# Optimization experiments

Measured on AMD Instinct MI355X. Metric: run time of the kernel, lower is better.

The kernel has to match this reference:

```python
import jax, jax.numpy as jnp
import numpy as np

N_NODES = 20000
N_EDGES = 320000
NUM_GRAPHS = 64
IN_DIM = 256


def setup_inputs() -> dict:
    key = jax.random.key(0)
    ks = jax.random.split(key, 12)
    x = jax.random.normal(ks[0], (N_NODES, IN_DIM), dtype=jnp.float32)
    edge_index = jax.random.randint(ks[1], (2, N_EDGES), 0, N_NODES, dtype=jnp.int64)
    batch = jnp.sort(jax.random.randint(ks[2], (N_NODES,), 0, NUM_GRAPHS, dtype=jnp.int64))
    def glorot(k, shape):
        lim = float(np.sqrt(6.0 / (shape[0] + shape[1])))
        return jax.random.uniform(k, shape, dtype=jnp.float32, minval=-lim, maxval=lim)
    W1 = glorot(ks[3], (IN_DIM, 256)); b1 = jnp.zeros((256,), jnp.float32)
    W2 = glorot(ks[4], (256, 128));   b2 = jnp.zeros((128,), jnp.float32)
    Wl1 = glorot(ks[5], (128, 64));   bl1 = jnp.zeros((64,), jnp.float32)
    Wl2 = glorot(ks[6], (64, 1));     bl2 = jnp.zeros((1,), jnp.float32)
    return {"x": x, "edge_index": edge_index, "batch": batch,
            "W1": W1, "b1": b1, "W2": W2, "b2": b2,
            "Wl1": Wl1, "bl1": bl1, "Wl2": Wl2, "bl2": bl2}


def gcn_conv(x, src, dst, W, b, n_nodes):
    # PyG GCNConv: add self-loops, symmetric normalization D^-1/2 (A+I) D^-1/2,
    # linear transform first, then gather-scale-scatter aggregation, then bias.
    loop = jnp.arange(n_nodes, dtype=src.dtype)
    s = jnp.concatenate([src, loop])
    d = jnp.concatenate([dst, loop])
    deg = jax.ops.segment_sum(jnp.ones_like(d, dtype=x.dtype), d, num_segments=n_nodes)
    dinv = jnp.where(deg > 0, jax.lax.rsqrt(deg), 0.0)
    norm = dinv[s] * dinv[d]                         # [E+N]
    h = x @ W                                        # [N, out]
    msg = h[s] * norm[:, None]                       # [E+N, out]
    out = jax.ops.segment_sum(msg, d, num_segments=n_nodes)
    return out + b


def global_mean_pool(x, batch, num_graphs):
    sums = jax.ops.segment_sum(x, batch, num_segments=num_graphs)
    cnts = jax.ops.segment_sum(jnp.ones((x.shape[0],), x.dtype), batch, num_segments=num_graphs)
    return sums / jnp.maximum(cnts, 1.0)[:, None]


def reference(x, edge_index, batch, W1, b1, W2, b2, Wl1, bl1, Wl2, bl2):
    n = x.shape[0]
    src, dst = edge_index[0], edge_index[1]
    h = jax.nn.relu(gcn_conv(x, src, dst, W1, b1, n))   # dropout = identity (eval)
    h = jax.nn.relu(gcn_conv(h, src, dst, W2, b2, n))
    g = global_mean_pool(h, batch, NUM_GRAPHS)          # [G, 128]
    g = jax.nn.relu(g @ Wl1 + bl1)
    return jax.nn.sigmoid(g @ Wl2 + bl2)                # [G, 1]
```

## Files before the change

kernel.cpp:

```cpp
#include <hip/hip_runtime.h>
#include <hip/hip_bf16.h>
#include <math.h>

typedef __attribute__((ext_vector_type(8))) short bf16x8;
typedef __attribute__((ext_vector_type(4))) float f32x4;

__device__ __forceinline__ unsigned short f2bf(float f) {
    unsigned int u = __float_as_uint(f);
    unsigned int r = (u + 0x7FFFu + ((u >> 16) & 1u)) >> 16;
    return (unsigned short)r;
}
__device__ __forceinline__ unsigned char f2fp8(float v) {
    int p = __builtin_amdgcn_cvt_pk_fp8_f32(v, v, 0, false);
    return (unsigned char)(p & 0xff);
}
__device__ __forceinline__ unsigned int pk4fp8(float a, float b, float c, float d) {
    int p = __builtin_amdgcn_cvt_pk_fp8_f32(a, b, 0, false);
    p = __builtin_amdgcn_cvt_pk_fp8_f32(c, d, p, true);
    return (unsigned int)p;
}
__device__ __forceinline__ void fp8x8_fma(uint2 u, float w, float* a) {
    a[0] += __builtin_amdgcn_cvt_f32_fp8((int)u.x, 0) * w;
    a[1] += __builtin_amdgcn_cvt_f32_fp8((int)u.x, 1) * w;
    a[2] += __builtin_amdgcn_cvt_f32_fp8((int)u.x, 2) * w;
    a[3] += __builtin_amdgcn_cvt_f32_fp8((int)u.x, 3) * w;
    a[4] += __builtin_amdgcn_cvt_f32_fp8((int)u.y, 0) * w;
    a[5] += __builtin_amdgcn_cvt_f32_fp8((int)u.y, 1) * w;
    a[6] += __builtin_amdgcn_cvt_f32_fp8((int)u.y, 2) * w;
    a[7] += __builtin_amdgcn_cvt_f32_fp8((int)u.y, 3) * w;
}
__device__ __forceinline__ void fp8x4_fma(unsigned int u, float w, float* a) {
    a[0] += __builtin_amdgcn_cvt_f32_fp8((int)u, 0) * w;
    a[1] += __builtin_amdgcn_cvt_f32_fp8((int)u, 1) * w;
    a[2] += __builtin_amdgcn_cvt_f32_fp8((int)u, 2) * w;
    a[3] += __builtin_amdgcn_cvt_f32_fp8((int)u, 3) * w;
}
__device__ __forceinline__ float deg_dinv(int c) { return rsqrtf((float)c + 1.0f); }

__device__ __forceinline__ void load_lds16(const unsigned short* g, unsigned short* l) {
    __builtin_amdgcn_global_load_lds(
        (const __attribute__((address_space(1))) unsigned int*)g,
        (__attribute__((address_space(3))) unsigned int*)l, 16, 0, 0);
}

__global__ __launch_bounds__(256) void prep_kernel(const float* __restrict__ x,
                                                   unsigned short* __restrict__ xh,
                                                   const int* __restrict__ batch,
                                                   int* __restrict__ gstart,
                                                   const float* __restrict__ W1,
                                                   unsigned short* __restrict__ w1t,
                                                   const float* __restrict__ W2,
                                                   unsigned short* __restrict__ w2t,
                                                   int N, int G, int CXB, int BNB) {
    int b = blockIdx.x;
    int tid = threadIdx.x;
    if (b < CXB) {
        size_t idx0 = ((size_t)b * 256 + tid) * 2;
        size_t total4 = (size_t)N * 64;
#pragma unroll
        for (int r = 0; r < 2; r++) {
            size_t idx = idx0 + r;
            if (idx < total4) {
                float4 v = ((const float4*)x)[idx];
                ushort4 o;
                o.x = f2bf(v.x); o.y = f2bf(v.y); o.z = f2bf(v.z); o.w = f2bf(v.w);
                ((ushort4*)xh)[idx] = o;
            }
        }
        return;
    }
    b -= CXB;
    if (b < BNB) {
        int i = b * 256 + tid;
        if (i >= N) return;
        int bb = batch[i];
        if (i == 0) { for (int g = 0; g <= bb; g++) gstart[g] = 0; }
        else { int bp = batch[i - 1]; for (int g = bp + 1; g <= bb; g++) gstart[g] = i; }
        if (i == N - 1) { for (int g = bb + 1; g <= G; g++) gstart[g] = N; }
        return;
    }
    b -= BNB;
    {
        int idx = b * 256 + tid;
        if (idx < 256 * 256) {
            int m = idx >> 8, k = idx & 255;
            w1t[idx] = f2bf(W1[(size_t)k * 256 + m]);
        } else if (idx < 256 * 256 + 128 * 256) {
            int j = idx - 256 * 256;
            int m = j >> 8, k = j & 255;
            w2t[j] = f2bf(W2[(size_t)k * 128 + m]);
        }
    }
}

__device__ __forceinline__ void gemm_body(const unsigned short* __restrict__ A,
                                          const unsigned short* __restrict__ Bt,
                                          unsigned char* __restrict__ C8,
                                          int N, int M, int bx, int by,
                                          unsigned short* As, unsigned short* Bs) {
    const int K = 256;
    int tid = threadIdx.x;
    int wave = tid >> 6, lane = tid & 63;
    int quad = lane >> 4, m16 = lane & 15;
    int r0 = by * 128, c0 = bx * 64;
    int srow = lane >> 2;
    int skoff = (lane & 3) * 8;

    f32x4 acc[2][4];
#pragma unroll
    for (int rg = 0; rg < 2; rg++)
#pragma unroll
        for (int ct = 0; ct < 4; ct++) acc[rg][ct] = (f32x4){0.f, 0.f, 0.f, 0.f};

    for (int kb = 0; kb < K; kb += 32) {
#pragma unroll
        for (int i = 0; i < 2; i++) {
            int brow = wave * 32 + i * 16 + srow;
            int grow = r0 + brow; if (grow >= N) grow = N - 1;
            load_lds16(A + (size_t)grow * K + kb + skoff, As + (wave * 32 + i * 16) * 32);
        }
        {
            int bcol = wave * 16 + srow;
            load_lds16(Bt + (size_t)(c0 + bcol) * K + kb + skoff, Bs + (wave * 16) * 32);
        }
        __syncthreads();
        bf16x8 af[2], bf[4];
#pragma unroll
        for (int rg = 0; rg < 2; rg++)
            af[rg] = *(const bf16x8*)(As + (wave * 32 + rg * 16 + m16) * 32 + quad * 8);
#pragma unroll
        for (int ct = 0; ct < 4; ct++)
            bf[ct] = *(const bf16x8*)(Bs + (ct * 16 + m16) * 32 + quad * 8);
#pragma unroll
        for (int rg = 0; rg < 2; rg++)
#pragma unroll
            for (int ct = 0; ct < 4; ct++)
                acc[rg][ct] = __builtin_amdgcn_mfma_f32_16x16x32_bf16(af[rg], bf[ct], acc[rg][ct], 0, 0, 0);
        __syncthreads();
    }
#pragma unroll
    for (int rg = 0; rg < 2; rg++) {
#pragma unroll
        for (int ct = 0; ct < 4; ct++) {
            int col = c0 + ct * 16 + m16;
#pragma unroll
            for (int r = 0; r < 4; r++) {
                int row = r0 + wave * 32 + rg * 16 + quad * 4 + r;
                if (row < N) C8[(size_t)row * M + col] = f2fp8(acc[rg][ct][r]);
            }
        }
    }
}

__global__ __launch_bounds__(256) void fill_gemm1_kernel(const int* __restrict__ src,
                                                         const int* __restrict__ dst,
                                                         int* __restrict__ cnt,
                                                         int* __restrict__ csr,
                                                         const unsigned short* __restrict__ A,
                                                         const unsigned short* __restrict__ Bt,
                                                         unsigned char* __restrict__ C8,
                                                         int N, int E, int FB) {
    __shared__ unsigned short As[128 * 32];
    __shared__ unsigned short Bs[64 * 32];
    if ((int)blockIdx.x < FB) {
        int e = (blockIdx.x * 256 + threadIdx.x) * 4;
        if (e + 3 < E) {
            int4 d4 = *(const int4*)(dst + e);
            int4 s4 = *(const int4*)(src + e);
            int sl;
            sl = atomicAdd(&cnt[d4.x], 1); if (sl < 64) csr[(d4.x << 6) + sl] = s4.x;
            sl = atomicAdd(&cnt[d4.y], 1); if (sl < 64) csr[(d4.y << 6) + sl] = s4.y;
            sl = atomicAdd(&cnt[d4.z], 1); if (sl < 64) csr[(d4.z << 6) + sl] = s4.z;
            sl = atomicAdd(&cnt[d4.w], 1); if (sl < 64) csr[(d4.w << 6) + sl] = s4.w;
        } else {
            for (; e < E; e++) {
                int d = dst[e];
                int slot = atomicAdd(&cnt[d], 1);
                if (slot < 64) csr[(d << 6) + slot] = src[e];
            }
        }
        return;
    }
    int gb = blockIdx.x - FB;
    gemm_body(A, Bt, C8, N, 256, gb & 3, gb >> 2, As, Bs);
}

__global__ __launch_bounds__(256) void gemm2_kernel(const unsigned short* __restrict__ A,
                                                    const unsigned short* __restrict__ Bt,
                                                    unsigned char* __restrict__ C8, int N) {
    __shared__ unsigned short As[128 * 32];
    __shared__ unsigned short Bs[64 * 32];
    gemm_body(A, Bt, C8, N, 128, blockIdx.x, blockIdx.y, As, Bs);
}

__global__ __launch_bounds__(256) void gather256_kernel(const unsigned char* __restrict__ h8,
                                                        const int* __restrict__ csr,
                                                        const int* __restrict__ cnt,
                                                        const float* __restrict__ bias,
                                                        unsigned short* __restrict__ out, int N) {
    int node = blockIdx.x * 4 + (threadIdx.x >> 6);
    if (node >= N) return;
    int lane = threadIdx.x & 63;
    int half = lane >> 5, hl = lane & 31;
    int beg = node << 6;
    int c = cnt[node]; if (c > 64) c = 64;
    int end = beg + c;
    float a[8] = {0, 0, 0, 0, 0, 0, 0, 0};
    int j = beg;
    for (; j + 7 < end; j += 8) {
        int s0 = csr[j + half], s1 = csr[j + 2 + half];
        int s2 = csr[j + 4 + half], s3 = csr[j + 6 + half];
        float w0 = deg_dinv(cnt[s0]), w1 = deg_dinv(cnt[s1]);
        float w2 = deg_dinv(cnt[s2]), w3 = deg_dinv(cnt[s3]);
        uint2 u0 = *(const uint2*)(h8 + (size_t)s0 * 256 + hl * 8);
        uint2 u1 = *(const uint2*)(h8 + (size_t)s1 * 256 + hl * 8);
        uint2 u2 = *(const uint2*)(h8 + (size_t)s2 * 256 + hl * 8);
        uint2 u3 = *(const uint2*)(h8 + (size_t)s3 * 256 + hl * 8);
        fp8x8_fma(u0, w0, a); fp8x8_fma(u1, w1, a);
        fp8x8_fma(u2, w2, a); fp8x8_fma(u3, w3, a);
    }
    for (; j + 1 < end; j += 2) {
        int s0 = csr[j + half];
        float w0 = deg_dinv(cnt[s0]);
        uint2 u0 = *(const uint2*)(h8 + (size_t)s0 * 256 + hl * 8);
        fp8x8_fma(u0, w0, a);
    }
    if (j < end && half == 0) {
        int s0 = csr[j];
        float w0 = deg_dinv(cnt[s0]);
        uint2 u0 = *(const uint2*)(h8 + (size_t)s0 * 256 + hl * 8);
        fp8x8_fma(u0, w0, a);
    }
#pragma unroll
    for (int i = 0; i < 8; i++) a[i] += __shfl_down(a[i], 32);
    if (half == 0) {
        float dd = deg_dinv(c);
        float self[8] = {0, 0, 0, 0, 0, 0, 0, 0};
        uint2 uh = *(const uint2*)(h8 + (size_t)node * 256 + hl * 8);
        fp8x8_fma(uh, dd, self);
        float4 bv0 = ((const float4*)bias)[hl * 2];
        float4 bv1 = ((const float4*)bias)[hl * 2 + 1];
        float bvf[8] = {bv0.x, bv0.y, bv0.z, bv0.w, bv1.x, bv1.y, bv1.z, bv1.w};
        bf16x8 o;
#pragma unroll
        for (int i = 0; i < 8; i++)
            o[i] = (short)f2bf(fmaxf((a[i] + self[i]) * dd + bvf[i], 0.f));
        ((bf16x8*)(out + (size_t)node * 256))[hl] = o;
    }
}

__global__ __launch_bounds__(256) void gather128_kernel(const unsigned char* __restrict__ t8,
                                                        const int* __restrict__ csr,
                                                        const int* __restrict__ cnt,
                                                        const float* __restrict__ bias,
                                                        unsigned char* __restrict__ out2, int N) {
    int node = blockIdx.x * 4 + (threadIdx.x >> 6);
    if (node >= N) return;
    int lane = threadIdx.x & 63;
    int half = lane >> 5, hl = lane & 31;
    int beg = node << 6;
    int c = cnt[node]; if (c > 64) c = 64;
    int end = beg + c;
    float a[4] = {0, 0, 0, 0};
    int j = beg;
    for (; j + 7 < end; j += 8) {
        int s0 = csr[j + half], s1 = csr[j + 2 + half];
        int s2 = csr[j + 4 + half], s3 = csr[j + 6 + half];
        float w0 = deg_dinv(cnt[s0]), w1 = deg_dinv(cnt[s1]);
        float w2 = deg_dinv(cnt[s2]), w3 = deg_dinv(cnt[s3]);
        unsigned int u0 = *(const unsigned int*)(t8 + (size_t)s0 * 128 + hl * 4);
        unsigned int u1 = *(const unsigned int*)(t8 + (size_t)s1 * 128 + hl * 4);
        unsigned int u2 = *(const unsigned int*)(t8 + (size_t)s2 * 128 + hl * 4);
        unsigned int u3 = *(const unsigned int*)(t8 + (size_t)s3 * 128 + hl * 4);
        fp8x4_fma(u0, w0, a); fp8x4_fma(u1, w1, a);
        fp8x4_fma(u2, w2, a); fp8x4_fma(u3, w3, a);
    }
    for (; j + 1 < end; j += 2) {
        int s0 = csr[j + half];
        float w0 = deg_dinv(cnt[s0]);
        unsigned int u0 = *(const unsigned int*)(t8 + (size_t)s0 * 128 + hl * 4);
        fp8x4_fma(u0, w0, a);
    }
    if (j < end && half == 0) {
        int s0 = csr[j];
        float w0 = deg_dinv(cnt[s0]);
        unsigned int u0 = *(const unsigned int*)(t8 + (size_t)s0 * 128 + hl * 4);
        fp8x4_fma(u0, w0, a);
    }
#pragma unroll
    for (int i = 0; i < 4; i++) a[i] += __shfl_down(a[i], 32);
    if (half == 0) {
        float dd = deg_dinv(c);
        float self[4] = {0, 0, 0, 0};
        unsigned int uh = *(const unsigned int*)(t8 + (size_t)node * 128 + hl * 4);
        fp8x4_fma(uh, dd, self);
        float4 bv = ((const float4*)bias)[hl];
        float r0 = fmaxf((a[0] + self[0]) * dd + bv.x, 0.f);
        float r1 = fmaxf((a[1] + self[1]) * dd + bv.y, 0.f);
        float r2 = fmaxf((a[2] + self[2]) * dd + bv.z, 0.f);
        float r3 = fmaxf((a[3] + self[3]) * dd + bv.w, 0.f);
        ((unsigned int*)(out2 + (size_t)node * 128))[hl] = pk4fp8(r0, r1, r2, r3);
    }
}

__global__ __launch_bounds__(256) void poolhead_kernel(const unsigned char* __restrict__ out2,
                                                       const int* __restrict__ gstart,
                                                       float* __restrict__ gsum,
                                                       int* __restrict__ gdone,
                                                       const float* __restrict__ Wl1,
                                                       const float* __restrict__ bl1,
                                                       const float* __restrict__ Wl2,
                                                       const float* __restrict__ bl2,
                                                       float* __restrict__ out) {
    int g = blockIdx.x >> 3, slice = blockIdx.x & 7;
    int tid = threadIdx.x;
    int hw = tid >> 5, hl = tid & 31;
    int gs = gstart[g], ge = gstart[g + 1];
    float a[4] = {0, 0, 0, 0};
    for (int i = gs + slice * 8 + hw; i < ge; i += 64) {
        unsigned int u = ((const unsigned int*)(out2 + (size_t)i * 128))[hl];
        fp8x4_fma(u, 1.0f, a);
    }
    __shared__ float red[8][128];
#pragma unroll
    for (int k = 0; k < 4; k++) red[hw][hl * 4 + k] = a[k];
    __syncthreads();
    if (tid < 128) {
        float s = 0.f;
#pragma unroll
        for (int w = 0; w < 8; w++) s += red[w][tid];
        if (s != 0.f) atomicAdd(&gsum[g * 128 + tid], s);
    }
    __syncthreads();
    __shared__ int lastflag;
    if (tid == 0) {
        __threadfence();
        int old = atomicAdd(&gdone[g], 1);
        lastflag = (old == 7) ? 1 : 0;
    }
    __syncthreads();
    if (!lastflag) return;
    __shared__ float gv[128];
    if (tid < 128) {
        float s = atomicAdd(&gsum[g * 128 + tid], 0.0f);
        float cntf = fmaxf((float)(ge - gs), 1.0f);
        gv[tid] = s / cntf;
    }
    __syncthreads();
    if (tid < 64) {
        float acc = bl1[tid];
#pragma unroll 8
        for (int k = 0; k < 128; k++) acc += gv[k] * Wl1[k * 64 + tid];
        acc = fmaxf(acc, 0.f);
        float p = acc * Wl2[tid];
#pragma unroll
        for (int off = 32; off; off >>= 1) p += __shfl_down(p, off);
        if (tid == 0) out[g] = 1.f / (1.f + expf(-(p + bl2[0])));
    }
}

extern "C" void kernel_launch(void* const* d_in, const int* in_sizes, int n_in,
                              void* d_out, int out_size, void* d_ws, size_t ws_size,
                              hipStream_t stream) {
    const float* x   = (const float*)d_in[0];
    const int* ei    = (const int*)d_in[1];
    const int* batch = (const int*)d_in[2];
    const float* W1  = (const float*)d_in[3];
    const float* b1  = (const float*)d_in[4];
    const float* W2  = (const float*)d_in[5];
    const float* b2  = (const float*)d_in[6];
    const float* Wl1 = (const float*)d_in[7];
    const float* bl1 = (const float*)d_in[8];
    const float* Wl2 = (const float*)d_in[9];
    const float* bl2 = (const float*)d_in[10];
    float* out = (float*)d_out;

    const int N = in_sizes[2];
    const int E = in_sizes[1] / 2;
    const int G = 64;
    const int* src = ei;
    const int* dst = ei + E;

    char* base = (char*)d_ws;
    size_t off = 0;
    auto carve = [&](size_t bytes) -> char* {
        char* p = base + off;
        off = (off + bytes + 15) & ~(size_t)15;
        return p;
    };
    int*   cnt    = (int*)carve((size_t)N * 4);
    float* gsum   = (float*)carve((size_t)G * 128 * 4);
    int*   gdone  = (int*)carve((size_t)G * 4);
    size_t zero_bytes = (size_t)(N + G * 128 + G) * 4 + 32;
    int*   csr    = (int*)carve((size_t)N * 64 * 4);
    int*   gstart = (int*)carve((size_t)(G + 1) * 4);
    unsigned short* w1t = (unsigned short*)carve((size_t)256 * 256 * 2);
    unsigned short* w2t = (unsigned short*)carve((size_t)128 * 256 * 2);
    unsigned short* xh  = (unsigned short*)carve((size_t)N * 256 * 2);
    unsigned char*  h8  = (unsigned char*)carve((size_t)N * 256);
    unsigned short* o1h = (unsigned short*)carve((size_t)N * 256 * 2);
    unsigned char* t8   = (unsigned char*)xh;
    unsigned char* out2 = h8;

    hipMemsetAsync(d_ws, 0, zero_bytes, stream);

    const int CXB = (int)(((size_t)N * 32 + 255) / 256);
    const int BNB = (N + 255) / 256;
    const int CWB = (256 * 256 + 128 * 256 + 255) / 256;
    prep_kernel<<<CXB + BNB + CWB, 256, 0, stream>>>(
        x, xh, batch, gstart, W1, w1t, W2, w2t, N, G, CXB, BNB);

    const int FB  = (E / 4 + 255) / 256;
    const int GB1 = 4 * ((N + 127) / 128);
    fill_gemm1_kernel<<<FB + GB1, 256, 0, stream>>>(src, dst, cnt, csr,
                                                    xh, w1t, h8, N, E, FB);

    gather256_kernel<<<(N + 3) / 4, 256, 0, stream>>>(h8, csr, cnt, b1, o1h, N);

    {
        dim3 grid(2, (N + 127) / 128);
        gemm2_kernel<<<grid, 256, 0, stream>>>(o1h, w2t, t8, N);
    }
    gather128_kernel<<<(N + 3) / 4, 256, 0, stream>>>(t8, csr, cnt, b2, out2, N);

    poolhead_kernel<<<G * 8, 256, 0, stream>>>(out2, gstart, gsum, gdone,
                                               Wl1, bl1, Wl2, bl2, out);
}
```

Measured before the change: 173.4 us.

## Fuse x conversion into GEMM1, use FP8 for layer-2 GEMM, fuse pooling into gather

Drops the separate fp32-to-bf16 pass over x. GEMM1 now reads fp32 x directly, converts it in registers and writes a swizzled LDS tile, with the output tile widened to 128 columns. Layer-1 output is stored as FP8 instead of bf16, and GEMM2 uses FP8 MFMA with half-size loads. The second gather is fused with mean pooling and the MLP head: per-graph partial sums are accumulated with atomics, and a per-graph completion counter lets the last block finish the head. This removes one kernel launch and a full pass over the activations, but adds more quantization error and atomic contention.

```diff
diff --git a/kernel.cpp b/kernel.cpp
--- a/kernel.cpp
+++ b/kernel.cpp
@@ -42,34 +42,21 @@
         (const __attribute__((address_space(1))) unsigned int*)g,
         (__attribute__((address_space(3))) unsigned int*)l, 16, 0, 0);
 }
-
-__global__ __launch_bounds__(256) void prep_kernel(const float* __restrict__ x,
-                                                   unsigned short* __restrict__ xh,
-                                                   const int* __restrict__ batch,
+__device__ __forceinline__ void load_lds16_u8(const unsigned char* g, unsigned char* l) {
+    __builtin_amdgcn_global_load_lds(
+        (const __attribute__((address_space(1))) unsigned int*)g,
+        (__attribute__((address_space(3))) unsigned int*)l, 16, 0, 0);
+}
+
+__global__ __launch_bounds__(256) void prep_kernel(const int* __restrict__ batch,
                                                    int* __restrict__ gstart,
                                                    const float* __restrict__ W1,
                                                    unsigned short* __restrict__ w1t,
                                                    const float* __restrict__ W2,
-                                                   unsigned short* __restrict__ w2t,
-                                                   int N, int G, int CXB, int BNB) {
+                                                   unsigned char* __restrict__ w2t8,
+                                                   int N, int G, int BNB) {
     int b = blockIdx.x;
     int tid = threadIdx.x;
-    if (b < CXB) {
-        size_t idx0 = ((size_t)b * 256 + tid) * 2;
-        size_t total4 = (size_t)N * 64;
-#pragma unroll
-        for (int r = 0; r < 2; r++) {
-            size_t idx = idx0 + r;
-            if (idx < total4) {
-                float4 v = ((const float4*)x)[idx];
-                ushort4 o;
-                o.x = f2bf(v.x); o.y = f2bf(v.y); o.z = f2bf(v.z); o.w = f2bf(v.w);
-                ((ushort4*)xh)[idx] = o;
-            }
-        }
-        return;
-    }
-    b -= CXB;
     if (b < BNB) {
         int i = b * 256 + tid;
         if (i >= N) return;
@@ -79,76 +66,14 @@
         if (i == N - 1) { for (int g = bb + 1; g <= G; g++) gstart[g] = N; }
         return;
     }
-    b -= BNB;
-    {
-        int idx = b * 256 + tid;
-        if (idx < 256 * 256) {
-            int m = idx >> 8, k = idx & 255;
-            w1t[idx] = f2bf(W1[(size_t)k * 256 + m]);
-        } else if (idx < 256 * 256 + 128 * 256) {
-            int j = idx - 256 * 256;
-            int m = j >> 8, k = j & 255;
-            w2t[j] = f2bf(W2[(size_t)k * 128 + m]);
-        }
-    }
-}
-
-__device__ __forceinline__ void gemm_body(const unsigned short* __restrict__ A,
-                                          const unsigned short* __restrict__ Bt,
-                                          unsigned char* __restrict__ C8,
-                                          int N, int M, int bx, int by,
-                                          unsigned short* As, unsigned short* Bs) {
-    const int K = 256;
-    int tid = threadIdx.x;
-    int wave = tid >> 6, lane = tid & 63;
-    int quad = lane >> 4, m16 = lane & 15;
-    int r0 = by * 128, c0 = bx * 64;
-    int srow = lane >> 2;
-    int skoff = (lane & 3) * 8;
-
-    f32x4 acc[2][4];
-#pragma unroll
-    for (int rg = 0; rg < 2; rg++)
-#pragma unroll
-        for (int ct = 0; ct < 4; ct++) acc[rg][ct] = (f32x4){0.f, 0.f, 0.f, 0.f};
-
-    for (int kb = 0; kb < K; kb += 32) {
-#pragma unroll
-        for (int i = 0; i < 2; i++) {
-            int brow = wave * 32 + i * 16 + srow;
-            int grow = r0 + brow; if (grow >= N) grow = N - 1;
-            load_lds16(A + (size_t)grow * K + kb + skoff, As + (wave * 32 + i * 16) * 32);
-        }
-        {
-            int bcol = wave * 16 + srow;
-            load_lds16(Bt + (size_t)(c0 + bcol) * K + kb + skoff, Bs + (wave * 16) * 32);
-        }
-        __syncthreads();
-        bf16x8 af[2], bf[4];
-#pragma unroll
-        for (int rg = 0; rg < 2; rg++)
-            af[rg] = *(const bf16x8*)(As + (wave * 32 + rg * 16 + m16) * 32 + quad * 8);
-#pragma unroll
-        for (int ct = 0; ct < 4; ct++)
-            bf[ct] = *(const bf16x8*)(Bs + (ct * 16 + m16) * 32 + quad * 8);
-#pragma unroll
-        for (int rg = 0; rg < 2; rg++)
-#pragma unroll
-            for (int ct = 0; ct < 4; ct++)
-                acc[rg][ct] = __builtin_amdgcn_mfma_f32_16x16x32_bf16(af[rg], bf[ct], acc[rg][ct], 0, 0, 0);
-        __syncthreads();
-    }
-#pragma unroll
-    for (int rg = 0; rg < 2; rg++) {
-#pragma unroll
-        for (int ct = 0; ct < 4; ct++) {
-            int col = c0 + ct * 16 + m16;
-#pragma unroll
-            for (int r = 0; r < 4; r++) {
-                int row = r0 + wave * 32 + rg * 16 + quad * 4 + r;
-                if (row < N) C8[(size_t)row * M + col] = f2fp8(acc[rg][ct][r]);
-            }
-        }
+    int idx = (b - BNB) * 256 + tid;
+    if (idx < 256 * 256) {
+        int m = idx >> 8, k = idx & 255;
+        w1t[idx] = f2bf(W1[(size_t)k * 256 + m]);
+    } else if (idx < 256 * 256 + 128 * 256) {
+        int j = idx - 256 * 256;
+        int m = j >> 8, k = j & 255;
+        w2t8[j] = f2fp8(W2[(size_t)k * 128 + m]);
     }
 }
 
@@ -156,12 +81,12 @@
                                                          const int* __restrict__ dst,
                                                          int* __restrict__ cnt,
                                                          int* __restrict__ csr,
-                                                         const unsigned short* __restrict__ A,
+                                                         const float* __restrict__ x,
                                                          const unsigned short* __restrict__ Bt,
                                                          unsigned char* __restrict__ C8,
                                                          int N, int E, int FB) {
     __shared__ unsigned short As[128 * 32];
-    __shared__ unsigned short Bs[64 * 32];
+    __shared__ unsigned short Bs[128 * 32];
     if ((int)blockIdx.x < FB) {
         int e = (blockIdx.x * 256 + threadIdx.x) * 4;
         if (e + 3 < E) {
@@ -182,22 +107,141 @@
         return;
     }
     int gb = blockIdx.x - FB;
-    gemm_body(A, Bt, C8, N, 256, gb & 3, gb >> 2, As, Bs);
-}
-
-__global__ __launch_bounds__(256) void gemm2_kernel(const unsigned short* __restrict__ A,
-                                                    const unsigned short* __restrict__ Bt,
+    int bx = gb & 1, by = gb >> 1;
+    const int K = 256;
+    int tid = threadIdx.x;
+    int wave = tid >> 6, lane = tid & 63;
+    int quad = lane >> 4, m16 = lane & 15;
+    int r0 = by * 128, c0 = bx * 128;
+    int srow = lane >> 2;
+    int skoff = (lane & 3) * 8;
+
+    f32x4 acc[2][8];
+#pragma unroll
+    for (int rg = 0; rg < 2; rg++)
+#pragma unroll
+        for (int ct = 0; ct < 8; ct++) acc[rg][ct] = (f32x4){0.f, 0.f, 0.f, 0.f};
+
+    int arow = tid >> 1, akh = tid & 1;
+    int agrow = r0 + arow; if (agrow >= N) agrow = N - 1;
+    const float* ap = x + (size_t)agrow * K + akh * 16;
+    int asw = (arow >> 1) & 3;
+    unsigned short* as0 = As + arow * 32 + ((((akh << 1) | 0) ^ asw) << 3);
+    unsigned short* as1 = As + arow * 32 + ((((akh << 1) | 1) ^ asw) << 3);
+    int rsw = (m16 >> 1) & 3;
+
+    for (int kb = 0; kb < K; kb += 32) {
+        float4 f0 = *(const float4*)(ap + kb);
+        float4 f1 = *(const float4*)(ap + kb + 4);
+        float4 f2 = *(const float4*)(ap + kb + 8);
+        float4 f3 = *(const float4*)(ap + kb + 12);
+        {
+            int bcol = wave * 16 + srow;
+            load_lds16(Bt + (size_t)(c0 + bcol) * K + kb + skoff, Bs + (wave * 16) * 32);
+            load_lds16(Bt + (size_t)(c0 + 64 + bcol) * K + kb + skoff, Bs + (64 + wave * 16) * 32);
+        }
+        bf16x8 u0, u1;
+        u0[0] = (short)f2bf(f0.x); u0[1] = (short)f2bf(f0.y);
+        u0[2] = (short)f2bf(f0.z); u0[3] = (short)f2bf(f0.w);
+        u0[4] = (short)f2bf(f1.x); u0[5] = (short)f2bf(f1.y);
+        u0[6] = (short)f2bf(f1.z); u0[7] = (short)f2bf(f1.w);
+        u1[0] = (short)f2bf(f2.x); u1[1] = (short)f2bf(f2.y);
+        u1[2] = (short)f2bf(f2.z); u1[3] = (short)f2bf(f2.w);
+        u1[4] = (short)f2bf(f3.x); u1[5] = (short)f2bf(f3.y);
+        u1[6] = (short)f2bf(f3.z); u1[7] = (short)f2bf(f3.w);
+        *(bf16x8*)as0 = u0;
+        *(bf16x8*)as1 = u1;
+        __syncthreads();
+        bf16x8 af[2], bfr[8];
+#pragma unroll
+        for (int rg = 0; rg < 2; rg++)
+            af[rg] = *(const bf16x8*)(As + (wave * 32 + rg * 16 + m16) * 32 + ((quad ^ rsw) << 3));
+#pragma unroll
+        for (int ct = 0; ct < 8; ct++)
+            bfr[ct] = *(const bf16x8*)(Bs + (ct * 16 + m16) * 32 + (quad << 3));
+#pragma unroll
+        for (int rg = 0; rg < 2; rg++)
+#pragma unroll
+            for (int ct = 0; ct < 8; ct++)
+                acc[rg][ct] = __builtin_amdgcn_mfma_f32_16x16x32_bf16(af[rg], bfr[ct], acc[rg][ct], 0, 0, 0);
+        __syncthreads();
+    }
+#pragma unroll
+    for (int rg = 0; rg < 2; rg++) {
+#pragma unroll
+        for (int ct = 0; ct < 8; ct++) {
+            int col = c0 + ct * 16 + m16;
+#pragma unroll
+            for (int r = 0; r < 4; r++) {
+                int row = r0 + wave * 32 + rg * 16 + quad * 4 + r;
+                if (row < N) C8[(size_t)row * 256 + col] = f2fp8(acc[rg][ct][r]);
+            }
+        }
+    }
+}
+
+__global__ __launch_bounds__(256) void gemm2_kernel(const unsigned char* __restrict__ A,
+                                                    const unsigned char* __restrict__ Bt,
                                                     unsigned char* __restrict__ C8, int N) {
-    __shared__ unsigned short As[128 * 32];
-    __shared__ unsigned short Bs[64 * 32];
-    gemm_body(A, Bt, C8, N, 128, blockIdx.x, blockIdx.y, As, Bs);
+    __shared__ unsigned char As8[128 * 32];
+    __shared__ unsigned char Bs8[64 * 32];
+    const int K = 256;
+    int tid = threadIdx.x;
+    int wave = tid >> 6, lane = tid & 63;
+    int quad = lane >> 4, m16 = lane & 15;
+    int bx = blockIdx.x, by = blockIdx.y;
+    int r0 = by * 128, c0 = bx * 64;
+
+    f32x4 acc[2][4];
+#pragma unroll
+    for (int rg = 0; rg < 2; rg++)
+#pragma unroll
+        for (int ct = 0; ct < 4; ct++) acc[rg][ct] = (f32x4){0.f, 0.f, 0.f, 0.f};
+
+    int arow = wave * 32 + (lane >> 1);
+    int agrow = r0 + arow; if (agrow >= N) agrow = N - 1;
+    int ach = (lane & 1) * 16;
+    int brow = (wave & 1) * 32 + (lane >> 1);
+    int bch = (lane & 1) * 16;
+
+    for (int kb = 0; kb < K; kb += 32) {
+        load_lds16_u8(A + (size_t)agrow * K + kb + ach, As8 + (wave * 32) * 32);
+        if (wave < 2)
+            load_lds16_u8(Bt + (size_t)(c0 + brow) * K + kb + bch, Bs8 + (wave * 32) * 32);
+        __syncthreads();
+        long af[2], bfr[4];
+#pragma unroll
+        for (int rg = 0; rg < 2; rg++)
+            af[rg] = *(const long*)(As8 + (wave * 32 + rg * 16 + m16) * 32 + (quad << 3));
+#pragma unroll
+        for (int ct = 0; ct < 4; ct++)
+            bfr[ct] = *(const long*)(Bs8 + (ct * 16 + m16) * 32 + (quad << 3));
+#pragma unroll
+        for (int rg = 0; rg < 2; rg++)
+#pragma unroll
+            for (int ct = 0; ct < 4; ct++)
+                acc[rg][ct] = __builtin_amdgcn_mfma_f32_16x16x32_fp8_fp8(af[rg], bfr[ct], acc[rg][ct], 0, 0, 0);
+        __syncthreads();
+    }
+#pragma unroll
+    for (int rg = 0; rg < 2; rg++) {
+#pragma unroll
+        for (int ct = 0; ct < 4; ct++) {
+            int col = c0 + ct * 16 + m16;
+#pragma unroll
+            for (int r = 0; r < 4; r++) {
+                int row = r0 + wave * 32 + rg * 16 + quad * 4 + r;
+                if (row < N) C8[(size_t)row * 128 + col] = f2fp8(acc[rg][ct][r]);
+            }
+        }
+    }
 }
 
 __global__ __launch_bounds__(256) void gather256_kernel(const unsigned char* __restrict__ h8,
                                                         const int* __restrict__ csr,
                                                         const int* __restrict__ cnt,
                                                         const float* __restrict__ bias,
-                                                        unsigned short* __restrict__ out, int N) {
+                                                        unsigned char* __restrict__ o18, int N) {
     int node = blockIdx.x * 4 + (threadIdx.x >> 6);
     if (node >= N) return;
     int lane = threadIdx.x & 63;
@@ -241,121 +285,152 @@
         float4 bv0 = ((const float4*)bias)[hl * 2];
         float4 bv1 = ((const float4*)bias)[hl * 2 + 1];
         float bvf[8] = {bv0.x, bv0.y, bv0.z, bv0.w, bv1.x, bv1.y, bv1.z, bv1.w};
-        bf16x8 o;
-#pragma unroll
-        for (int i = 0; i < 8; i++)
-            o[i] = (short)f2bf(fmaxf((a[i] + self[i]) * dd + bvf[i], 0.f));
-        ((bf16x8*)(out + (size_t)node * 256))[hl] = o;
-    }
-}
-
-__global__ __launch_bounds__(256) void gather128_kernel(const unsigned char* __restrict__ t8,
-                                                        const int* __restrict__ csr,
-                                                        const int* __restrict__ cnt,
-                                                        const float* __restrict__ bias,
-                                                        unsigned char* __restrict__ out2, int N) {
-    int node = blockIdx.x * 4 + (threadIdx.x >> 6);
-    if (node >= N) return;
-    int lane = threadIdx.x & 63;
+        float v[8];
+#pragma unroll
+        for (int i = 0; i < 8; i++) v[i] = fmaxf((a[i] + self[i]) * dd + bvf[i], 0.f);
+        uint2 o;
+        o.x = pk4fp8(v[0], v[1], v[2], v[3]);
+        o.y = pk4fp8(v[4], v[5], v[6], v[7]);
+        ((uint2*)(o18 + (size_t)node * 256))[hl] = o;
+    }
+}
+
+__global__ __launch_bounds__(256) void gather128ph_kernel(const unsigned char* __restrict__ t8,
+                                                          const int* __restrict__ csr,
+                                                          const int* __restrict__ cnt,
+                                                          const float* __restrict__ bias,
+                                                          const int* __restrict__ batch,
+                                                          const int* __restrict__ gstart,
+                                                          float* __restrict__ gsum,
+                                                          int* __restrict__ gdone,
+                                                          const float* __restrict__ Wl1,
+                                                          const float* __restrict__ bl1,
+                                                          const float* __restrict__ Wl2,
+                                                          const float* __restrict__ bl2,
+                                                          float* __restrict__ out, int N) {
+    int tid = threadIdx.x;
+    int nw = tid >> 6;
+    int node = blockIdx.x * 4 + nw;
+    int lane = tid & 63;
     int half = lane >> 5, hl = lane & 31;
-    int beg = node << 6;
-    int c = cnt[node]; if (c > 64) c = 64;
-    int end = beg + c;
-    float a[4] = {0, 0, 0, 0};
-    int j = beg;
-    for (; j + 7 < end; j += 8) {
-        int s0 = csr[j + half], s1 = csr[j + 2 + half];
-        int s2 = csr[j + 4 + half], s3 = csr[j + 6 + half];
-        float w0 = deg_dinv(cnt[s0]), w1 = deg_dinv(cnt[s1]);
-        float w2 = deg_dinv(cnt[s2]), w3 = deg_dinv(cnt[s3]);
-        unsigned int u0 = *(const unsigned int*)(t8 + (size_t)s0 * 128 + hl * 4);
-        unsigned int u1 = *(const unsigned int*)(t8 + (size_t)s1 * 128 + hl * 4);
-        unsigned int u2 = *(const unsigned int*)(t8 + (size_t)s2 * 128 + hl * 4);
-        unsigned int u3 = *(const unsigned int*)(t8 + (size_t)s3 * 128 + hl * 4);
-        fp8x4_fma(u0, w0, a); fp8x4_fma(u1, w1, a);
-        fp8x4_fma(u2, w2, a); fp8x4_fma(u3, w3, a);
-    }
-    for (; j + 1 < end; j += 2) {
-        int s0 = csr[j + half];
-        float w0 = deg_dinv(cnt[s0]);
-        unsigned int u0 = *(const unsigned int*)(t8 + (size_t)s0 * 128 + hl * 4);
-        fp8x4_fma(u0, w0, a);
-    }
-    if (j < end && half == 0) {
-        int s0 = csr[j];
-        float w0 = deg_dinv(cnt[s0]);
-        unsigned int u0 = *(const unsigned int*)(t8 + (size_t)s0 * 128 + hl * 4);
-        fp8x4_fma(u0, w0, a);
-    }
-#pragma unroll
-    for (int i = 0; i < 4; i++) a[i] += __shfl_down(a[i], 32);
-    if (half == 0) {
-        float dd = deg_dinv(c);
-        float self[4] = {0, 0, 0, 0};
-        unsigned int uh = *(const unsigned int*)(t8 + (size_t)node * 128 + hl * 4);
-        fp8x4_fma(uh, dd, self);
-        float4 bv = ((const float4*)bias)[hl];
-        float r0 = fmaxf((a[0] + self[0]) * dd + bv.x, 0.f);
-        float r1 = fmaxf((a[1] + self[1]) * dd + bv.y, 0.f);
-        float r2 = fmaxf((a[2] + self[2]) * dd + bv.z, 0.f);
-        float r3 = fmaxf((a[3] + self[3]) * dd + bv.w, 0.f);
-        ((unsigned int*)(out2 + (size_t)node * 128))[hl] = pk4fp8(r0, r1, r2, r3);
-    }
-}
-
-__global__ __launch_bounds__(256) void poolhead_kernel(const unsigned char* __restrict__ out2,
-                                                       const int* __restrict__ gstart,
-                                                       float* __restrict__ gsum,
-                                                       int* __restrict__ gdone,
-                                                       const float* __restrict__ Wl1,
-                                                       const float* __restrict__ bl1,
-                                                       const float* __restrict__ Wl2,
-                                                       const float* __restrict__ bl2,
-                                                       float* __restrict__ out) {
-    int g = blockIdx.x >> 3, slice = blockIdx.x & 7;
-    int tid = threadIdx.x;
-    int hw = tid >> 5, hl = tid & 31;
-    int gs = gstart[g], ge = gstart[g + 1];
-    float a[4] = {0, 0, 0, 0};
-    for (int i = gs + slice * 8 + hw; i < ge; i += 64) {
-        unsigned int u = ((const unsigned int*)(out2 + (size_t)i * 128))[hl];
-        fp8x4_fma(u, 1.0f, a);
-    }
-    __shared__ float red[8][128];
-#pragma unroll
-    for (int k = 0; k < 4; k++) red[hw][hl * 4 + k] = a[k];
+    bool valid = node < N;
+
+    __shared__ float red[4][128];
+    __shared__ int gid[4];
+    __shared__ int fg[4];
+    __shared__ int nf;
+    __shared__ float gv[128];
+
+    if (valid) {
+        int beg = node << 6;
+        int c = cnt[node]; if (c > 64) c = 64;
+        int end = beg + c;
+        float a[4] = {0, 0, 0, 0};
+        int j = beg;
+        for (; j + 7 < end; j += 8) {
+            int s0 = csr[j + half], s1 = csr[j + 2 + half];
+            int s2 = csr[j + 4 + half], s3 = csr[j + 6 + half];
+            float w0 = deg_dinv(cnt[s0]), w1 = deg_dinv(cnt[s1]);
+            float w2 = deg_dinv(cnt[s2]), w3 = deg_dinv(cnt[s3]);
+            unsigned int u0 = *(const unsigned int*)(t8 + (size_t)s0 * 128 + hl * 4);
+            unsigned int u1 = *(const unsigned int*)(t8 + (size_t)s1 * 128 + hl * 4);
+            unsigned int u2 = *(const unsigned int*)(t8 + (size_t)s2 * 128 + hl * 4);
+            unsigned int u3 = *(const unsigned int*)(t8 + (size_t)s3 * 128 + hl * 4);
+            fp8x4_fma(u0, w0, a); fp8x4_fma(u1, w1, a);
+            fp8x4_fma(u2, w2, a); fp8x4_fma(u3, w3, a);
+        }
+        for (; j + 1 < end; j += 2) {
+            int s0 = csr[j + half];
+            float w0 = deg_dinv(cnt[s0]);
+            unsigned int u0 = *(const unsigned int*)(t8 + (size_t)s0 * 128 + hl * 4);
+            fp8x4_fma(u0, w0, a);
+        }
+        if (j < end && half == 0) {
+            int s0 = csr[j];
+            float w0 = deg_dinv(cnt[s0]);
+            unsigned int u0 = *(const unsigned int*)(t8 + (size_t)s0 * 128 + hl * 4);
+            fp8x4_fma(u0, w0, a);
+        }
+#pragma unroll
+        for (int i = 0; i < 4; i++) a[i] += __shfl_down(a[i], 32);
+        if (lane == 0) gid[nw] = batch[node];
+        if (half == 0) {
+            float dd = deg_dinv(c);
+            float self[4] = {0, 0, 0, 0};
+            unsigned int uh = *(const unsigned int*)(t8 + (size_t)node * 128 + hl * 4);
+            fp8x4_fma(uh, dd, self);
+            float4 bv = ((const float4*)bias)[hl];
+            red[nw][hl * 4 + 0] = fmaxf((a[0] + self[0]) * dd + bv.x, 0.f);
+            red[nw][hl * 4 + 1] = fmaxf((a[1] + self[1]) * dd + bv.y, 0.f);
+            red[nw][hl * 4 + 2] = fmaxf((a[2] + self[2]) * dd + bv.z, 0.f);
+            red[nw][hl * 4 + 3] = fmaxf((a[3] + self[3]) * dd + bv.w, 0.f);
+        }
+    } else {
+        if (lane == 0) gid[nw] = -1;
+    }
     __syncthreads();
     if (tid < 128) {
-        float s = 0.f;
-#pragma unroll
-        for (int w = 0; w < 8; w++) s += red[w][tid];
-        if (s != 0.f) atomicAdd(&gsum[g * 128 + tid], s);
+        float s = 0.f; int gp = -1;
+#pragma unroll
+        for (int n = 0; n < 4; n++) {
+            int g = gid[n];
+            if (g < 0) continue;
+            if (g != gp) {
+                if (gp >= 0 && s != 0.f) atomicAdd(&gsum[gp * 128 + tid], s);
+                s = 0.f; gp = g;
+            }
+            s += red[n][tid];
+        }
+        if (gp >= 0 && s != 0.f) atomicAdd(&gsum[gp * 128 + tid], s);
     }
     __syncthreads();
-    __shared__ int lastflag;
     if (tid == 0) {
+        nf = 0;
         __threadfence();
-        int old = atomicAdd(&gdone[g], 1);
-        lastflag = (old == 7) ? 1 : 0;
+        int n = 0;
+        while (n < 4) {
+            int g = gid[n];
+            if (g < 0) { n++; continue; }
+            int len = 1;
+            while (n + len < 4 && gid[n + len] == g) len++;
+            int tot = gstart[g + 1] - gstart[g];
+            int old = atomicAdd(&gdone[g], len);
+            if (old + len == tot) fg[nf++] = g;
+            n += len;
+        }
     }
     __syncthreads();
-    if (!lastflag) return;
-    __shared__ float gv[128];
-    if (tid < 128) {
-        float s = atomicAdd(&gsum[g * 128 + tid], 0.0f);
-        float cntf = fmaxf((float)(ge - gs), 1.0f);
-        gv[tid] = s / cntf;
-    }
-    __syncthreads();
-    if (tid < 64) {
-        float acc = bl1[tid];
+    int nfl = nf;
+    for (int f = 0; f < nfl; f++) {
+        int g = fg[f];
+        if (tid < 128) {
+            float s = atomicAdd(&gsum[g * 128 + tid], 0.0f);
+            float cf = fmaxf((float)(gstart[g + 1] - gstart[g]), 1.0f);
+            gv[tid] = s / cf;
+        }
+        __syncthreads();
+        if (tid < 64) {
+            float acc = bl1[tid];
 #pragma unroll 8
-        for (int k = 0; k < 128; k++) acc += gv[k] * Wl1[k * 64 + tid];
-        acc = fmaxf(acc, 0.f);
-        float p = acc * Wl2[tid];
-#pragma unroll
-        for (int off = 32; off; off >>= 1) p += __shfl_down(p, off);
-        if (tid == 0) out[g] = 1.f / (1.f + expf(-(p + bl2[0])));
+            for (int k = 0; k < 128; k++) acc += gv[k] * Wl1[k * 64 + tid];
+            acc = fmaxf(acc, 0.f);
+            float p = acc * Wl2[tid];
+#pragma unroll
+            for (int off = 32; off; off >>= 1) p += __shfl_down(p, off);
+            if (tid == 0) out[g] = 1.f / (1.f + expf(-(p + bl2[0])));
+        }
+        __syncthreads();
+    }
+    if (blockIdx.x == 0 && tid < 64) {
+        for (int g = 0; g < 64; g++) {
+            if (gstart[g + 1] == gstart[g]) {
+                float acc = fmaxf(bl1[tid], 0.f);
+                float p = acc * Wl2[tid];
+#pragma unroll
+                for (int off = 32; off; off >>= 1) p += __shfl_down(p, off);
+                if (tid == 0) out[g] = 1.f / (1.f + expf(-(p + bl2[0])));
+            }
+        }
     }
 }
 
@@ -394,35 +469,30 @@
     size_t zero_bytes = (size_t)(N + G * 128 + G) * 4 + 32;
     int*   csr    = (int*)carve((size_t)N * 64 * 4);
     int*   gstart = (int*)carve((size_t)(G + 1) * 4);
-    unsigned short* w1t = (unsigned short*)carve((size_t)256 * 256 * 2);
-    unsigned short* w2t = (unsigned short*)carve((size_t)128 * 256 * 2);
-    unsigned short* xh  = (unsigned short*)carve((size_t)N * 256 * 2);
-    unsigned char*  h8  = (unsigned char*)carve((size_t)N * 256);
-    unsigned short* o1h = (unsigned short*)carve((size_t)N * 256 * 2);
-    unsigned char* t8   = (unsigned char*)xh;
-    unsigned char* out2 = h8;
+    unsigned short* w1t  = (unsigned short*)carve((size_t)256 * 256 * 2);
+    unsigned char*  w2t8 = (unsigned char*)carve((size_t)128 * 256);
+    unsigned char*  h8   = (unsigned char*)carve((size_t)N * 256);
+    unsigned char*  o18  = (unsigned char*)carve((size_t)N * 256);
+    unsigned char*  t8   = h8;
 
     hipMemsetAsync(d_ws, 0, zero_bytes, stream);
 
-    const int CXB = (int)(((size_t)N * 32 + 255) / 256);
     const int BNB = (N + 255) / 256;
     const int CWB = (256 * 256 + 128 * 256 + 255) / 256;
-    prep_kernel<<<CXB + BNB + CWB, 256, 0, stream>>>(
-        x, xh, batch, gstart, W1, w1t, W2, w2t, N, G, CXB, BNB);
+    prep_kernel<<<BNB + CWB, 256, 0, stream>>>(batch, gstart, W1, w1t, W2, w2t8, N, G, BNB);
 
     const int FB  = (E / 4 + 255) / 256;
-    const int GB1 = 4 * ((N + 127) / 128);
+    const int GB1 = 2 * ((N + 127) / 128);
     fill_gemm1_kernel<<<FB + GB1, 256, 0, stream>>>(src, dst, cnt, csr,
-                                                    xh, w1t, h8, N, E, FB);
-
-    gather256_kernel<<<(N + 3) / 4, 256, 0, stream>>>(h8, csr, cnt, b1, o1h, N);
+                                                    x, w1t, h8, N, E, FB);
+
+    gather256_kernel<<<(N + 3) / 4, 256, 0, stream>>>(h8, csr, cnt, b1, o18, N);
 
     {
         dim3 grid(2, (N + 127) / 128);
-        gemm2_kernel<<<grid, 256, 0, stream>>>(o1h, w2t, t8, N);
-    }
-    gather128_kernel<<<(N + 3) / 4, 256, 0, stream>>>(t8, csr, cnt, b2, out2, N);
-
-    poolhead_kernel<<<G * 8, 256, 0, stream>>>(out2, gstart, gsum, gdone,
-                                               Wl1, bl1, Wl2, bl2, out);
-}
+        gemm2_kernel<<<grid, 256, 0, stream>>>(o18, w2t8, t8, N);
+    }
+
+    gather128ph_kernel<<<(N + 3) / 4, 256, 0, stream>>>(t8, csr, cnt, b2, batch, gstart,
+                                                        gsum, gdone, Wl1, bl1, Wl2, bl2, out, N);
+}
```

New measurement: 244.9 us. 1.41x slower.
